# Optimization experiments

Measured on AMD Instinct MI355X. Metric: run time of the kernel, lower is better.

## Reference

```python
import jax, jax.numpy as jnp
import numpy as np
from jax import lax

HIDDEN = 256
CONV = 128
DIST = 11
GRID = DIST + 1            # 12
N_STAB = DIST * DIST - 1   # 120
N_LAYERS = 2
DILATIONS = tuple(min(2 ** i, DIST) for i in range(N_LAYERS))  # (1, 2)
EPS = 1e-5

# row-major placement of the first N_STAB grid cells (matches _build_grid_maps)
ROWS = jnp.arange(N_STAB) // GRID
COLS = jnp.arange(N_STAB) % GRID


def setup_inputs() -> dict:
    key = jax.random.key(0)
    ks = jax.random.split(key, 12)
    s_in = 1.0 / np.sqrt(HIDDEN)
    s_cv = 1.0 / np.sqrt(CONV * 9)
    s_out = 1.0 / np.sqrt(CONV)
    return {
        "x": jax.random.normal(ks[0], (4096, N_STAB, HIDDEN), jnp.float32),
        "W_in": jax.random.uniform(ks[1], (HIDDEN, CONV), jnp.float32, -s_in, s_in),
        "b_in": jax.random.uniform(ks[2], (CONV,), jnp.float32, -s_in, s_in),
        "conv_w": jax.random.uniform(ks[3], (N_LAYERS, CONV, CONV, 3, 3), jnp.float32, -s_cv, s_cv),
        "conv_b": jax.random.uniform(ks[4], (N_LAYERS, CONV), jnp.float32, -s_cv, s_cv),
        "bn_g": jnp.ones((N_LAYERS, CONV), jnp.float32),
        "bn_b": jnp.zeros((N_LAYERS, CONV), jnp.float32),
        "W_out": jax.random.uniform(ks[5], (CONV, HIDDEN), jnp.float32, -s_out, s_out),
        "b_out": jax.random.uniform(ks[6], (HIDDEN,), jnp.float32, -s_out, s_out),
        "ln_g": jnp.ones((HIDDEN,), jnp.float32),
        "ln_b": jnp.zeros((HIDDEN,), jnp.float32),
    }


def _dilated_conv(g, w, b, dil):
    # g: [B, C, G, G], w: [O, I, 3, 3]
    y = lax.conv_general_dilated(
        g, w, window_strides=(1, 1),
        padding=((dil, dil), (dil, dil)),
        rhs_dilation=(dil, dil),
        dimension_numbers=("NCHW", "OIHW", "NCHW"))
    return y + b[None, :, None, None]


def _batchnorm_train(y, gamma, beta):
    # training-mode BN: batch stats over (N, H, W), biased variance
    mean = jnp.mean(y, axis=(0, 2, 3), keepdims=True)
    var = jnp.mean(jnp.square(y - mean), axis=(0, 2, 3), keepdims=True)
    yhat = (y - mean) * lax.rsqrt(var + EPS)
    return yhat * gamma[None, :, None, None] + beta[None, :, None, None]


def reference(x, W_in, b_in, conv_w, conv_b, bn_g, bn_b, W_out, b_out, ln_g, ln_b):
    B = x.shape[0]
    # proj_in: [B, S, H] -> [B, S, C]
    h = jnp.einsum("bsh,hc->bsc", x, W_in) + b_in
    # scatter to grid: [B, C, G, G]
    grid = jnp.zeros((B, CONV, GRID, GRID), dtype=h.dtype)
    grid = grid.at[:, :, ROWS, COLS].set(jnp.transpose(h, (0, 2, 1)))
    for i, dil in enumerate(DILATIONS):
        y = _dilated_conv(grid, conv_w[i], conv_b[i], dil)
        grid = grid + jax.nn.relu(_batchnorm_train(y, bn_g[i], bn_b[i]))
    # gather back: [B, S, C]
    h = jnp.transpose(grid[:, :, ROWS, COLS], (0, 2, 1))
    # proj_out + residual + LayerNorm
    h = jnp.einsum("bsc,ch->bsh", h, W_out) + b_out
    z = x + h
    mu = jnp.mean(z, axis=-1, keepdims=True)
    var = jnp.mean(jnp.square(z - mu), axis=-1, keepdims=True)
    return (z - mu) * lax.rsqrt(var + EPS) * ln_g + ln_b
```

## Files before the change

### kernel.cpp

```cpp
#include <hip/hip_runtime.h>

typedef __attribute__((ext_vector_type(8))) unsigned short u16x8;
typedef __attribute__((ext_vector_type(8))) __bf16 bf16x8;
typedef __attribute__((ext_vector_type(4))) float f32x4;

#define DEVINL __device__ __forceinline__

DEVINL f32x4 MF(u16x8 a, u16x8 b, f32x4 c) {
  return __builtin_amdgcn_mfma_f32_16x16x32_bf16(
      __builtin_bit_cast(bf16x8, a), __builtin_bit_cast(bf16x8, b), c, 0, 0, 0);
}
DEVINL unsigned short f2b(float f) {
  return __builtin_bit_cast(unsigned short, (__bf16)f);
}
DEVINL float b2f(unsigned short h) {
  unsigned u = ((unsigned)h) << 16;
  return __builtin_bit_cast(float, u);
}

__global__ void k_prep(const float* __restrict__ W_in, const float* __restrict__ conv_w,
                       const float* __restrict__ W_out, unsigned short* __restrict__ Wt_in,
                       unsigned short* __restrict__ Wc, unsigned short* __restrict__ Wt_out) {
  int t = blockIdx.x * 256 + threadIdx.x;
  if (t < 128 * 256) { int c = t >> 8, h = t & 255; Wt_in[t] = f2b(W_in[h * 128 + c]); }
  if (t < 256 * 128) { int h = t >> 7, c = t & 127; Wt_out[t] = f2b(W_out[c * 256 + h]); }
  for (int i = t; i < 2 * 9 * 128 * 128; i += 65536) {
    int ii = i & 127, o = (i >> 7) & 127, rest = i >> 14;
    int kk = rest % 9, L = rest / 9;
    Wc[i] = f2b(conv_w[(size_t)((L * 128 + o) * 128 + ii) * 9 + kk]);
  }
}

DEVINL void conv_body(const char* GT, const unsigned short* __restrict__ WcL,
                      const float* __restrict__ convbL, int dil,
                      unsigned short* __restrict__ ybp, float* __restrict__ partials,
                      int b, int w, int hi, int lo) {
  const f32x4 Z = {0.f, 0.f, 0.f, 0.f};
  f32x4 acc[9][2];
#pragma unroll
  for (int mt = 0; mt < 9; ++mt) { acc[mt][0] = Z; acc[mt][1] = Z; }

  int pr[9], pc[9];
#pragma unroll
  for (int mt = 0; mt < 9; ++mt) {
    int p = mt * 16 + lo;
    pr[mt] = p / 12;
    pc[mt] = p - pr[mt] * 12;
  }

  for (int off = 0; off < 9; ++off) {
    const int dh = (off / 3 - 1) * dil, dw = (off % 3 - 1) * dil;
    int rb[9], sz[9];
#pragma unroll
    for (int mt = 0; mt < 9; ++mt) {
      int r2 = pr[mt] + dh, c2 = pc[mt] + dw;
      bool ok = ((unsigned)r2 < 12u) && ((unsigned)c2 < 12u);
      int ps = ok ? (r2 * 12 + c2) : 144;
      rb[mt] = ps * 256;
      sz[mt] = (ps & 7) << 4;
    }
    const unsigned short* Ao = WcL + off * (128 * 128);
#pragma unroll
    for (int ks = 0; ks < 4; ++ks) {
      const int kb = ks * 32 + hi * 8;
      u16x8 b0 = *(const u16x8*)(Ao + (w * 32 + lo) * 128 + kb);
      u16x8 b1 = *(const u16x8*)(Ao + (w * 32 + 16 + lo) * 128 + kb);
#pragma unroll
      for (int mt = 0; mt < 9; ++mt) {
        u16x8 a = *(const u16x8*)(GT + rb[mt] + ((kb * 2) ^ sz[mt]));
        acc[mt][0] = MF(a, b0, acc[mt][0]);
        acc[mt][1] = MF(a, b1, acc[mt][1]);
      }
    }
  }

  const float bias0 = convbL[w * 32 + lo], bias1 = convbL[w * 32 + 16 + lo];
  float s1a = 0.f, s2a = 0.f, s1b = 0.f, s2b = 0.f;
#pragma unroll
  for (int mt = 0; mt < 9; ++mt)
#pragma unroll
    for (int r = 0; r < 4; ++r) {
      const int p = mt * 16 + hi * 4 + r;
      float ya = acc[mt][0][r] + bias0;
      float yb = acc[mt][1][r] + bias1;
      s1a += ya; s2a += ya * ya; s1b += yb; s2b += yb * yb;
      ybp[p * 128 + w * 32 + lo]      = f2b(ya);
      ybp[p * 128 + w * 32 + 16 + lo] = f2b(yb);
    }
  s1a += __shfl_xor(s1a, 16); s1a += __shfl_xor(s1a, 32);
  s2a += __shfl_xor(s2a, 16); s2a += __shfl_xor(s2a, 32);
  s1b += __shfl_xor(s1b, 16); s1b += __shfl_xor(s1b, 32);
  s2b += __shfl_xor(s2b, 16); s2b += __shfl_xor(s2b, 32);
  if (hi == 0) {
    const int o0 = w * 32 + lo;
    partials[(size_t)o0 * 4096 + b]              = s1a;
    partials[(size_t)(128 + o0) * 4096 + b]      = s2a;
    partials[(size_t)(o0 + 16) * 4096 + b]       = s1b;
    partials[(size_t)(128 + o0 + 16) * 4096 + b] = s2b;
  }
}

__global__ __launch_bounds__(256) void k_in(
    const float* __restrict__ x, const unsigned short* __restrict__ Wt_in,
    const float* __restrict__ b_in, const unsigned short* __restrict__ Wc0,
    const float* __restrict__ convb0, unsigned short* __restrict__ gridb,
    unsigned short* __restrict__ ybuf, float* __restrict__ partials) {
  __shared__ unsigned short Gt[145 * 128];
  char* GT = (char*)Gt;
  const int b = blockIdx.x, t = threadIdx.x;
  const int l = t & 63, hi = l >> 4, lo = l & 15, w = t >> 6;
  const float* xb = x + (size_t)b * 120 * 256;

  const f32x4 Z = {0.f, 0.f, 0.f, 0.f};
  f32x4 acc[2][8];
#pragma unroll
  for (int mi = 0; mi < 2; ++mi)
#pragma unroll
    for (int cn = 0; cn < 8; ++cn) acc[mi][cn] = Z;

#pragma unroll
  for (int ks = 0; ks < 8; ++ks) {
    const int kb = ks * 32 + hi * 8;
    u16x8 af[2];
#pragma unroll
    for (int mi = 0; mi < 2; ++mi) {
      int s = w * 32 + mi * 16 + lo;
      s = s < 120 ? s : 119;
      const float* px = xb + s * 256 + kb;
      f32x4 v0 = *(const f32x4*)px;
      f32x4 v1 = *(const f32x4*)(px + 4);
      u16x8 a;
#pragma unroll
      for (int j = 0; j < 4; ++j) { a[j] = f2b(v0[j]); a[4 + j] = f2b(v1[j]); }
      af[mi] = a;
    }
#pragma unroll
    for (int cn = 0; cn < 8; ++cn) {
      u16x8 bf = *(const u16x8*)(Wt_in + (cn * 16 + lo) * 256 + kb);
      acc[0][cn] = MF(af[0], bf, acc[0][cn]);
      acc[1][cn] = MF(af[1], bf, acc[1][cn]);
    }
  }

  float binr[8];
#pragma unroll
  for (int cn = 0; cn < 8; ++cn) binr[cn] = b_in[cn * 16 + lo];

#pragma unroll
  for (int mi = 0; mi < 2; ++mi)
#pragma unroll
    for (int r = 0; r < 4; ++r) {
      const int s = w * 32 + mi * 16 + hi * 4 + r;
      if (s < 120) {
        const int sw = (s & 7) << 4;
#pragma unroll
        for (int cn = 0; cn < 8; ++cn) {
          const int cb = (cn * 16 + lo) * 2;
          *(unsigned short*)(GT + s * 256 + (cb ^ sw)) = f2b(acc[mi][cn][r] + binr[cn]);
        }
      }
    }
  {
    u16x8 zz = {0, 0, 0, 0, 0, 0, 0, 0};
    for (int idx = t; idx < 25 * 16; idx += 256) {
      int row = 120 + (idx >> 4), ch = (idx & 15) << 4;
      *(u16x8*)(GT + row * 256 + (ch ^ ((row & 7) << 4))) = zz;
    }
  }
  __syncthreads();

  unsigned short* gbp = gridb + (size_t)b * 144 * 128;
  for (int idx = t; idx < 144 * 16; idx += 256) {
    int row = idx >> 4, ch = (idx & 15) << 4;
    u16x8 v = *(const u16x8*)(GT + row * 256 + (ch ^ ((row & 7) << 4)));
    *(u16x8*)(gbp + row * 128 + ((idx & 15) << 3)) = v;
  }

  conv_body(GT, Wc0, convb0, 1, ybuf + (size_t)b * 144 * 128, partials, b, w, hi, lo);
}

__global__ __launch_bounds__(256) void k_conv2(
    unsigned short* __restrict__ gridb, unsigned short* __restrict__ ybuf,
    const float* __restrict__ statsP, const unsigned short* __restrict__ WcL,
    const float* __restrict__ convbL, float* __restrict__ partials) {
  __shared__ unsigned short Gt[145 * 128];
  char* GT = (char*)Gt;
  const int b = blockIdx.x, t = threadIdx.x;
  unsigned short* gbp = gridb + (size_t)b * 144 * 128;
  unsigned short* ybp = ybuf + (size_t)b * 144 * 128;
  const int c0 = (t & 15) * 8, prow = t >> 4;
  const f32x4 a0 = *(const f32x4*)(statsP + c0);
  const f32x4 a1 = *(const f32x4*)(statsP + c0 + 4);
  const f32x4 g0 = *(const f32x4*)(statsP + 128 + c0);
  const f32x4 g1 = *(const f32x4*)(statsP + 128 + c0 + 4);

#pragma unroll
  for (int it = 0; it < 9; ++it) {
    const int p = prow + 16 * it;
    u16x8 g = *(const u16x8*)(gbp + p * 128 + c0);
    u16x8 y = *(const u16x8*)(ybp + p * 128 + c0);
    u16x8 o;
#pragma unroll
    for (int j = 0; j < 4; ++j) {
      o[j]     = f2b(b2f(g[j])     + fmaxf(0.f, b2f(y[j])     * a0[j] + g0[j]));
      o[4 + j] = f2b(b2f(g[4 + j]) + fmaxf(0.f, b2f(y[4 + j]) * a1[j] + g1[j]));
    }
    *(u16x8*)(gbp + p * 128 + c0) = o;
    *(u16x8*)(GT + p * 256 + ((c0 * 2) ^ ((p & 7) << 4))) = o;
  }
  if (t < 16) {
    u16x8 zz = {0, 0, 0, 0, 0, 0, 0, 0};
    *(u16x8*)(GT + 144 * 256 + t * 16) = zz;
  }
  __syncthreads();

  conv_body(GT, WcL, convbL, 2, ybp, partials, b, t >> 6, (t & 63) >> 4, t & 15);
}

__global__ void k_stats(const float* __restrict__ partials, const float* __restrict__ bn_g,
                        const float* __restrict__ bn_b, float* __restrict__ statsL, float invN) {
  const int c = blockIdx.x, t = threadIdx.x;
  float s1 = 0.f, s2 = 0.f;
  const float* p1 = partials + (size_t)c * 4096;
  const float* p2 = partials + (size_t)(128 + c) * 4096;
  for (int j = t; j < 4096; j += 256) { s1 += p1[j]; s2 += p2[j]; }
#pragma unroll
  for (int m = 1; m < 64; m <<= 1) { s1 += __shfl_xor(s1, m); s2 += __shfl_xor(s2, m); }
  __shared__ float r1[4], r2[4];
  if ((t & 63) == 0) { r1[t >> 6] = s1; r2[t >> 6] = s2; }
  __syncthreads();
  if (t == 0) {
    float S1 = r1[0] + r1[1] + r1[2] + r1[3];
    float S2 = r2[0] + r2[1] + r2[2] + r2[3];
    float mean = S1 * invN;
    float var = fmaxf(S2 * invN - mean * mean, 0.f);
    float a = bn_g[c] * rsqrtf(var + 1e-5f);
    statsL[c] = a;
    statsL[128 + c] = bn_b[c] - mean * a;
  }
}

__global__ __launch_bounds__(512) void k_out(
    const unsigned short* __restrict__ gridb, const unsigned short* __restrict__ ybuf,
    const float* __restrict__ statsP, const unsigned short* __restrict__ Wt_out,
    const float* __restrict__ b_out, const float* __restrict__ x,
    const float* __restrict__ ln_g, const float* __restrict__ ln_b,
    float* __restrict__ out) {
  __shared__ unsigned short Gs[128 * 128];
  char* GT = (char*)Gs;
  const int b = blockIdx.x, t = threadIdx.x;
  const unsigned short* gbp = gridb + (size_t)b * 144 * 128;
  const unsigned short* ybp = ybuf + (size_t)b * 144 * 128;
  const int c0 = (t & 15) * 8, prow = t >> 4;
  const f32x4 a0 = *(const f32x4*)(statsP + c0);
  const f32x4 a1 = *(const f32x4*)(statsP + c0 + 4);
  const f32x4 g0 = *(const f32x4*)(statsP + 128 + c0);
  const f32x4 g1 = *(const f32x4*)(statsP + 128 + c0 + 4);

#pragma unroll
  for (int it = 0; it < 4; ++it) {
    const int p = prow + 32 * it;
    u16x8 o = {0, 0, 0, 0, 0, 0, 0, 0};
    if (p < 120) {
      u16x8 g = *(const u16x8*)(gbp + p * 128 + c0);
      u16x8 y = *(const u16x8*)(ybp + p * 128 + c0);
#pragma unroll
      for (int j = 0; j < 4; ++j) {
        o[j]     = f2b(b2f(g[j])     + fmaxf(0.f, b2f(y[j])     * a0[j] + g0[j]));
        o[4 + j] = f2b(b2f(g[4 + j]) + fmaxf(0.f, b2f(y[4 + j]) * a1[j] + g1[j]));
      }
    }
    *(u16x8*)(GT + p * 256 + ((c0 * 2) ^ ((p & 7) << 4))) = o;
  }
  __syncthreads();

  const int l = t & 63, hi = l >> 4, lo = l & 15, w = t >> 6;
  const f32x4 Z = {0.f, 0.f, 0.f, 0.f};
  f32x4 acc[16];
#pragma unroll
  for (int nt = 0; nt < 16; ++nt) acc[nt] = Z;

#pragma unroll
  for (int ks = 0; ks < 4; ++ks) {
    const int kb = ks * 32 + hi * 8;
    const int r0 = w * 16 + lo;
    u16x8 A0 = *(const u16x8*)(GT + r0 * 256 + ((kb * 2) ^ ((r0 & 7) << 4)));
#pragma unroll
    for (int q = 0; q < 4; ++q)
#pragma unroll
      for (int j = 0; j < 4; ++j) {
        const int R = q * 64 + lo * 4 + j;
        u16x8 bf = *(const u16x8*)(Wt_out + R * 128 + kb);
        acc[q * 4 + j] = MF(A0, bf, acc[q * 4 + j]);
      }
  }

  const float* xb = x + (size_t)b * 120 * 256;
  float* ob = out + (size_t)b * 120 * 256;
  f32x4 bo4[4];
#pragma unroll
  for (int q = 0; q < 4; ++q) bo4[q] = *(const f32x4*)(b_out + q * 64 + lo * 4);

#pragma unroll
  for (int r = 0; r < 4; ++r) {
    const int row = w * 16 + hi * 4 + r;
    if (row < 120) {
      float s1 = 0.f, s2 = 0.f;
#pragma unroll
      for (int q = 0; q < 4; ++q) {
        f32x4 xv = *(const f32x4*)(xb + row * 256 + q * 64 + lo * 4);
#pragma unroll
        for (int j = 0; j < 4; ++j) {
          float v = acc[q * 4 + j][r] + bo4[q][j] + xv[j];
          acc[q * 4 + j][r] = v;
          s1 += v; s2 += v * v;
        }
      }
#pragma unroll
      for (int m = 1; m < 16; m <<= 1) { s1 += __shfl_xor(s1, m); s2 += __shfl_xor(s2, m); }
      const float mu = s1 * (1.f / 256.f);
      const float var = fmaxf(s2 * (1.f / 256.f) - mu * mu, 0.f);
      const float rs = rsqrtf(var + 1e-5f);
#pragma unroll
      for (int q = 0; q < 4; ++q) {
        f32x4 lg = *(const f32x4*)(ln_g + q * 64 + lo * 4);
        f32x4 lb = *(const f32x4*)(ln_b + q * 64 + lo * 4);
        f32x4 o4;
#pragma unroll
        for (int j = 0; j < 4; ++j)
          o4[j] = (acc[q * 4 + j][r] - mu) * rs * lg[j] + lb[j];
        *(f32x4*)(ob + row * 256 + q * 64 + lo * 4) = o4;
      }
    }
  }
}

extern "C" void kernel_launch(void* const* d_in, const int* in_sizes, int n_in,
                              void* d_out, int out_size, void* d_ws, size_t ws_size,
                              hipStream_t stream) {
  (void)in_sizes; (void)n_in; (void)out_size; (void)ws_size;
  const float* x      = (const float*)d_in[0];
  const float* W_in   = (const float*)d_in[1];
  const float* b_in   = (const float*)d_in[2];
  const float* conv_w = (const float*)d_in[3];
  const float* conv_b = (const float*)d_in[4];
  const float* bn_g   = (const float*)d_in[5];
  const float* bn_b   = (const float*)d_in[6];
  const float* W_out  = (const float*)d_in[7];
  const float* b_out  = (const float*)d_in[8];
  const float* ln_g   = (const float*)d_in[9];
  const float* ln_b   = (const float*)d_in[10];

  char* ws = (char*)d_ws;
  size_t off = 0;
  auto alloc = [&](size_t bytes) { char* p = ws + off; off = (off + bytes + 255) & ~(size_t)255; return p; };
  unsigned short* Wt_in  = (unsigned short*)alloc(128 * 256 * 2);
  unsigned short* Wc     = (unsigned short*)alloc(2 * 9 * 128 * 128 * 2);
  unsigned short* Wt_out = (unsigned short*)alloc(256 * 128 * 2);
  float* stats           = (float*)alloc(2 * 256 * 4);
  float* partials        = (float*)alloc((size_t)256 * 4096 * 4);
  unsigned short* gridb  = (unsigned short*)alloc((size_t)4096 * 144 * 128 * 2);
  unsigned short* ybuf   = (unsigned short*)alloc((size_t)4096 * 144 * 128 * 2);

  const float invN = 1.f / (4096.f * 144.f);

  k_prep<<<256, 256, 0, stream>>>(W_in, conv_w, W_out, Wt_in, Wc, Wt_out);
  k_in<<<4096, 256, 0, stream>>>(x, Wt_in, b_in, Wc, conv_b, gridb, ybuf, partials);
  k_stats<<<128, 256, 0, stream>>>(partials, bn_g, bn_b, stats, invN);
  k_conv2<<<4096, 256, 0, stream>>>(gridb, ybuf, stats, Wc + 9 * 128 * 128, conv_b + 128, partials);
  k_stats<<<128, 256, 0, stream>>>(partials, bn_g + 128, bn_b + 128, stats + 256, invN);
  k_out<<<4096, 512, 0, stream>>>(gridb, ybuf, stats + 256, Wt_out, b_out, x, ln_g, ln_b, (float*)d_out);
}
```

Before: 1.139 ms.

## Split k_out into one-wave blocks per 16-row tile for finer scheduling

```diff
diff --git a/kernel.cpp b/kernel.cpp
--- a/kernel.cpp
+++ b/kernel.cpp
@@ -240,41 +240,54 @@
   }
 }
 
-__global__ __launch_bounds__(512) void k_out(
+__global__ __launch_bounds__(64, 4) void k_out(
     const unsigned short* __restrict__ gridb, const unsigned short* __restrict__ ybuf,
     const float* __restrict__ statsP, const unsigned short* __restrict__ Wt_out,
     const float* __restrict__ b_out, const float* __restrict__ x,
     const float* __restrict__ ln_g, const float* __restrict__ ln_b,
     float* __restrict__ out) {
-  __shared__ unsigned short Gs[128 * 128];
+  __shared__ unsigned short Gs[16 * 128];
   char* GT = (char*)Gs;
-  const int b = blockIdx.x, t = threadIdx.x;
+  const int bid = blockIdx.x;
+  const int b = bid >> 3, blk = bid & 7;
   const unsigned short* gbp = gridb + (size_t)b * 144 * 128;
   const unsigned short* ybp = ybuf + (size_t)b * 144 * 128;
-  const int c0 = (t & 15) * 8, prow = t >> 4;
-  const f32x4 a0 = *(const f32x4*)(statsP + c0);
-  const f32x4 a1 = *(const f32x4*)(statsP + c0 + 4);
-  const f32x4 g0 = *(const f32x4*)(statsP + 128 + c0);
-  const f32x4 g1 = *(const f32x4*)(statsP + 128 + c0 + 4);
-
-#pragma unroll
-  for (int it = 0; it < 4; ++it) {
-    const int p = prow + 32 * it;
-    u16x8 o = {0, 0, 0, 0, 0, 0, 0, 0};
+  const int t = threadIdx.x;
+
+  {
+    const int p_loc = t >> 2, c0 = (t & 3) * 32;
+    const int p = blk * 16 + p_loc;
+    const int sw = (p_loc & 7) << 4;
     if (p < 120) {
-      u16x8 g = *(const u16x8*)(gbp + p * 128 + c0);
-      u16x8 y = *(const u16x8*)(ybp + p * 128 + c0);
 #pragma unroll
       for (int j = 0; j < 4; ++j) {
-        o[j]     = f2b(b2f(g[j])     + fmaxf(0.f, b2f(y[j])     * a0[j] + g0[j]));
-        o[4 + j] = f2b(b2f(g[4 + j]) + fmaxf(0.f, b2f(y[4 + j]) * a1[j] + g1[j]));
-      }
-    }
-    *(u16x8*)(GT + p * 256 + ((c0 * 2) ^ ((p & 7) << 4))) = o;
+        const int c = c0 + j * 8;
+        u16x8 g = *(const u16x8*)(gbp + p * 128 + c);
+        u16x8 y = *(const u16x8*)(ybp + p * 128 + c);
+        const f32x4 a0 = *(const f32x4*)(statsP + c);
+        const f32x4 a1 = *(const f32x4*)(statsP + c + 4);
+        const f32x4 g0 = *(const f32x4*)(statsP + 128 + c);
+        const f32x4 g1 = *(const f32x4*)(statsP + 128 + c + 4);
+        u16x8 o;
+#pragma unroll
+        for (int k = 0; k < 4; ++k) {
+          o[k]     = f2b(b2f(g[k])     + fmaxf(0.f, b2f(y[k])     * a0[k] + g0[k]));
+          o[4 + k] = f2b(b2f(g[4 + k]) + fmaxf(0.f, b2f(y[4 + k]) * a1[k] + g1[k]));
+        }
+        *(u16x8*)(GT + p_loc * 256 + ((c * 2) ^ sw)) = o;
+      }
+    } else {
+      u16x8 zz = {0, 0, 0, 0, 0, 0, 0, 0};
+#pragma unroll
+      for (int j = 0; j < 4; ++j) {
+        const int c = c0 + j * 8;
+        *(u16x8*)(GT + p_loc * 256 + ((c * 2) ^ sw)) = zz;
+      }
+    }
   }
   __syncthreads();
 
-  const int l = t & 63, hi = l >> 4, lo = l & 15, w = t >> 6;
+  const int hi = t >> 4, lo = t & 15;
   const f32x4 Z = {0.f, 0.f, 0.f, 0.f};
   f32x4 acc[16];
 #pragma unroll
@@ -283,8 +296,7 @@
 #pragma unroll
   for (int ks = 0; ks < 4; ++ks) {
     const int kb = ks * 32 + hi * 8;
-    const int r0 = w * 16 + lo;
-    u16x8 A0 = *(const u16x8*)(GT + r0 * 256 + ((kb * 2) ^ ((r0 & 7) << 4)));
+    u16x8 A0 = *(const u16x8*)(GT + lo * 256 + ((kb * 2) ^ ((lo & 7) << 4)));
 #pragma unroll
     for (int q = 0; q < 4; ++q)
 #pragma unroll
@@ -303,7 +315,7 @@
 
 #pragma unroll
   for (int r = 0; r < 4; ++r) {
-    const int row = w * 16 + hi * 4 + r;
+    const int row = blk * 16 + hi * 4 + r;
     if (row < 120) {
       float s1 = 0.f, s2 = 0.f;
 #pragma unroll
@@ -369,5 +381,5 @@
   k_stats<<<128, 256, 0, stream>>>(partials, bn_g, bn_b, stats, invN);
   k_conv2<<<4096, 256, 0, stream>>>(gridb, ybuf, stats, Wc + 9 * 128 * 128, conv_b + 128, partials);
   k_stats<<<128, 256, 0, stream>>>(partials, bn_g + 128, bn_b + 128, stats + 256, invN);
-  k_out<<<4096, 512, 0, stream>>>(gridb, ybuf, stats + 256, Wt_out, b_out, x, ln_g, ln_b, (float*)d_out);
-}
+  k_out<<<4096 * 8, 64, 0, stream>>>(gridb, ybuf, stats + 256, Wt_out, b_out, x, ln_g, ln_b, (float*)d_out);
+}
```

Measured after the change: 1.136 ms. About the same (-0.3%).

## Recompute conv outputs in later kernels instead of storing intermediate buffers

Applied to the files above, without the earlier changes.

```diff
diff --git a/kernel.cpp b/kernel.cpp
--- a/kernel.cpp
+++ b/kernel.cpp
@@ -31,10 +31,10 @@
   }
 }
 
-DEVINL void conv_body(const char* GT, const unsigned short* __restrict__ WcL,
+template <int YMODE, bool PART>
+DEVINL void conv_body(const char* GT, char* YL, const unsigned short* __restrict__ WcL,
                       const float* __restrict__ convbL, int dil,
-                      unsigned short* __restrict__ ybp, float* __restrict__ partials,
-                      int b, int w, int hi, int lo) {
+                      float* __restrict__ partials, int b, int w, int hi, int lo) {
   const f32x4 Z = {0.f, 0.f, 0.f, 0.f};
   f32x4 acc[9][2];
 #pragma unroll
@@ -83,20 +83,61 @@
       const int p = mt * 16 + hi * 4 + r;
       float ya = acc[mt][0][r] + bias0;
       float yb = acc[mt][1][r] + bias1;
-      s1a += ya; s2a += ya * ya; s1b += yb; s2b += yb * yb;
-      ybp[p * 128 + w * 32 + lo]      = f2b(ya);
-      ybp[p * 128 + w * 32 + 16 + lo] = f2b(yb);
-    }
-  s1a += __shfl_xor(s1a, 16); s1a += __shfl_xor(s1a, 32);
-  s2a += __shfl_xor(s2a, 16); s2a += __shfl_xor(s2a, 32);
-  s1b += __shfl_xor(s1b, 16); s1b += __shfl_xor(s1b, 32);
-  s2b += __shfl_xor(s2b, 16); s2b += __shfl_xor(s2b, 32);
-  if (hi == 0) {
-    const int o0 = w * 32 + lo;
-    partials[(size_t)o0 * 4096 + b]              = s1a;
-    partials[(size_t)(128 + o0) * 4096 + b]      = s2a;
-    partials[(size_t)(o0 + 16) * 4096 + b]       = s1b;
-    partials[(size_t)(128 + o0 + 16) * 4096 + b] = s2b;
+      if (PART) { s1a += ya; s2a += ya * ya; s1b += yb; s2b += yb * yb; }
+      if (YMODE == 1) {
+        const int sw = (p & 7) << 4;
+        *(unsigned short*)(YL + p * 256 + ((((w * 32 + lo) * 2)) ^ sw))      = f2b(ya);
+        *(unsigned short*)(YL + p * 256 + ((((w * 32 + 16 + lo) * 2)) ^ sw)) = f2b(yb);
+      }
+    }
+  if (PART) {
+    s1a += __shfl_xor(s1a, 16); s1a += __shfl_xor(s1a, 32);
+    s2a += __shfl_xor(s2a, 16); s2a += __shfl_xor(s2a, 32);
+    s1b += __shfl_xor(s1b, 16); s1b += __shfl_xor(s1b, 32);
+    s2b += __shfl_xor(s2b, 16); s2b += __shfl_xor(s2b, 32);
+    if (hi == 0) {
+      const int o0 = w * 32 + lo;
+      partials[(size_t)o0 * 4096 + b]              = s1a;
+      partials[(size_t)(128 + o0) * 4096 + b]      = s2a;
+      partials[(size_t)(o0 + 16) * 4096 + b]       = s1b;
+      partials[(size_t)(128 + o0 + 16) * 4096 + b] = s2b;
+    }
+  }
+}
+
+DEVINL void stage_grid(const unsigned short* __restrict__ gbp, char* GT, int t) {
+  const int c0 = (t & 15) * 8, prow = t >> 4;
+#pragma unroll
+  for (int it = 0; it < 9; ++it) {
+    const int p = prow + 16 * it;
+    u16x8 g = *(const u16x8*)(gbp + p * 128 + c0);
+    *(u16x8*)(GT + p * 256 + ((c0 * 2) ^ ((p & 7) << 4))) = g;
+  }
+  if (t < 16) {
+    u16x8 zz = {0, 0, 0, 0, 0, 0, 0, 0};
+    *(u16x8*)(GT + 144 * 256 + t * 16) = zz;
+  }
+}
+
+DEVINL void bn_apply(char* GT, const char* YL, const float* __restrict__ statsP, int t) {
+  const int c0 = (t & 15) * 8, prow = t >> 4;
+  const f32x4 a0 = *(const f32x4*)(statsP + c0);
+  const f32x4 a1 = *(const f32x4*)(statsP + c0 + 4);
+  const f32x4 g0 = *(const f32x4*)(statsP + 128 + c0);
+  const f32x4 g1 = *(const f32x4*)(statsP + 128 + c0 + 4);
+#pragma unroll
+  for (int it = 0; it < 9; ++it) {
+    const int p = prow + 16 * it;
+    const int ad = p * 256 + ((c0 * 2) ^ ((p & 7) << 4));
+    u16x8 g = *(const u16x8*)(GT + ad);
+    u16x8 y = *(const u16x8*)(YL + ad);
+    u16x8 o;
+#pragma unroll
+    for (int j = 0; j < 4; ++j) {
+      o[j]     = f2b(b2f(g[j])     + fmaxf(0.f, b2f(y[j])     * a0[j] + g0[j]));
+      o[4 + j] = f2b(b2f(g[4 + j]) + fmaxf(0.f, b2f(y[4 + j]) * a1[j] + g1[j]));
+    }
+    *(u16x8*)(GT + ad) = o;
   }
 }
 
@@ -104,7 +145,7 @@
     const float* __restrict__ x, const unsigned short* __restrict__ Wt_in,
     const float* __restrict__ b_in, const unsigned short* __restrict__ Wc0,
     const float* __restrict__ convb0, unsigned short* __restrict__ gridb,
-    unsigned short* __restrict__ ybuf, float* __restrict__ partials) {
+    float* __restrict__ partials) {
   __shared__ unsigned short Gt[145 * 128];
   char* GT = (char*)Gt;
   const int b = blockIdx.x, t = threadIdx.x;
@@ -176,45 +217,28 @@
     *(u16x8*)(gbp + row * 128 + ((idx & 15) << 3)) = v;
   }
 
-  conv_body(GT, Wc0, convb0, 1, ybuf + (size_t)b * 144 * 128, partials, b, w, hi, lo);
-}
-
-__global__ __launch_bounds__(256) void k_conv2(
-    unsigned short* __restrict__ gridb, unsigned short* __restrict__ ybuf,
-    const float* __restrict__ statsP, const unsigned short* __restrict__ WcL,
-    const float* __restrict__ convbL, float* __restrict__ partials) {
+  conv_body<0, true>(GT, nullptr, Wc0, convb0, 1, partials, b, w, hi, lo);
+}
+
+__global__ __launch_bounds__(256) void k_mid(
+    const unsigned short* __restrict__ gridb, const float* __restrict__ stats1,
+    const unsigned short* __restrict__ Wc0, const float* __restrict__ convb0,
+    const unsigned short* __restrict__ Wc1, const float* __restrict__ convb1,
+    float* __restrict__ partials) {
   __shared__ unsigned short Gt[145 * 128];
+  __shared__ unsigned short Yl[144 * 128];
   char* GT = (char*)Gt;
+  char* YL = (char*)Yl;
   const int b = blockIdx.x, t = threadIdx.x;
-  unsigned short* gbp = gridb + (size_t)b * 144 * 128;
-  unsigned short* ybp = ybuf + (size_t)b * 144 * 128;
-  const int c0 = (t & 15) * 8, prow = t >> 4;
-  const f32x4 a0 = *(const f32x4*)(statsP + c0);
-  const f32x4 a1 = *(const f32x4*)(statsP + c0 + 4);
-  const f32x4 g0 = *(const f32x4*)(statsP + 128 + c0);
-  const f32x4 g1 = *(const f32x4*)(statsP + 128 + c0 + 4);
-
-#pragma unroll
-  for (int it = 0; it < 9; ++it) {
-    const int p = prow + 16 * it;
-    u16x8 g = *(const u16x8*)(gbp + p * 128 + c0);
-    u16x8 y = *(const u16x8*)(ybp + p * 128 + c0);
-    u16x8 o;
-#pragma unroll
-    for (int j = 0; j < 4; ++j) {
-      o[j]     = f2b(b2f(g[j])     + fmaxf(0.f, b2f(y[j])     * a0[j] + g0[j]));
-      o[4 + j] = f2b(b2f(g[4 + j]) + fmaxf(0.f, b2f(y[4 + j]) * a1[j] + g1[j]));
-    }
-    *(u16x8*)(gbp + p * 128 + c0) = o;
-    *(u16x8*)(GT + p * 256 + ((c0 * 2) ^ ((p & 7) << 4))) = o;
-  }
-  if (t < 16) {
-    u16x8 zz = {0, 0, 0, 0, 0, 0, 0, 0};
-    *(u16x8*)(GT + 144 * 256 + t * 16) = zz;
-  }
-  __syncthreads();
-
-  conv_body(GT, WcL, convbL, 2, ybp, partials, b, t >> 6, (t & 63) >> 4, t & 15);
+  const int l = t & 63, hi = l >> 4, lo = l & 15, w = t >> 6;
+
+  stage_grid(gridb + (size_t)b * 144 * 128, GT, t);
+  __syncthreads();
+  conv_body<1, false>(GT, YL, Wc0, convb0, 1, nullptr, b, w, hi, lo);
+  __syncthreads();
+  bn_apply(GT, YL, stats1, t);
+  __syncthreads();
+  conv_body<0, true>(GT, nullptr, Wc1, convb1, 2, partials, b, w, hi, lo);
 }
 
 __global__ void k_stats(const float* __restrict__ partials, const float* __restrict__ bn_g,
@@ -240,58 +264,53 @@
   }
 }
 
-__global__ __launch_bounds__(512) void k_out(
-    const unsigned short* __restrict__ gridb, const unsigned short* __restrict__ ybuf,
-    const float* __restrict__ statsP, const unsigned short* __restrict__ Wt_out,
-    const float* __restrict__ b_out, const float* __restrict__ x,
-    const float* __restrict__ ln_g, const float* __restrict__ ln_b,
-    float* __restrict__ out) {
-  __shared__ unsigned short Gs[128 * 128];
-  char* GT = (char*)Gs;
+__global__ __launch_bounds__(256) void k_out(
+    const unsigned short* __restrict__ gridb, const float* __restrict__ stats1,
+    const float* __restrict__ stats2,
+    const unsigned short* __restrict__ Wc0, const float* __restrict__ convb0,
+    const unsigned short* __restrict__ Wc1, const float* __restrict__ convb1,
+    const unsigned short* __restrict__ Wt_out, const float* __restrict__ b_out,
+    const float* __restrict__ x, const float* __restrict__ ln_g,
+    const float* __restrict__ ln_b, float* __restrict__ out) {
+  __shared__ unsigned short Gt[145 * 128];
+  __shared__ unsigned short Yl[144 * 128];
+  char* GT = (char*)Gt;
+  char* YL = (char*)Yl;
   const int b = blockIdx.x, t = threadIdx.x;
-  const unsigned short* gbp = gridb + (size_t)b * 144 * 128;
-  const unsigned short* ybp = ybuf + (size_t)b * 144 * 128;
-  const int c0 = (t & 15) * 8, prow = t >> 4;
-  const f32x4 a0 = *(const f32x4*)(statsP + c0);
-  const f32x4 a1 = *(const f32x4*)(statsP + c0 + 4);
-  const f32x4 g0 = *(const f32x4*)(statsP + 128 + c0);
-  const f32x4 g1 = *(const f32x4*)(statsP + 128 + c0 + 4);
-
-#pragma unroll
-  for (int it = 0; it < 4; ++it) {
-    const int p = prow + 32 * it;
-    u16x8 o = {0, 0, 0, 0, 0, 0, 0, 0};
-    if (p < 120) {
-      u16x8 g = *(const u16x8*)(gbp + p * 128 + c0);
-      u16x8 y = *(const u16x8*)(ybp + p * 128 + c0);
-#pragma unroll
-      for (int j = 0; j < 4; ++j) {
-        o[j]     = f2b(b2f(g[j])     + fmaxf(0.f, b2f(y[j])     * a0[j] + g0[j]));
-        o[4 + j] = f2b(b2f(g[4 + j]) + fmaxf(0.f, b2f(y[4 + j]) * a1[j] + g1[j]));
-      }
-    }
-    *(u16x8*)(GT + p * 256 + ((c0 * 2) ^ ((p & 7) << 4))) = o;
-  }
-  __syncthreads();
-
   const int l = t & 63, hi = l >> 4, lo = l & 15, w = t >> 6;
+
+  stage_grid(gridb + (size_t)b * 144 * 128, GT, t);
+  __syncthreads();
+  conv_body<1, false>(GT, YL, Wc0, convb0, 1, nullptr, b, w, hi, lo);
+  __syncthreads();
+  bn_apply(GT, YL, stats1, t);
+  __syncthreads();
+  conv_body<1, false>(GT, YL, Wc1, convb1, 2, nullptr, b, w, hi, lo);
+  __syncthreads();
+  bn_apply(GT, YL, stats2, t);
+  __syncthreads();
+
   const f32x4 Z = {0.f, 0.f, 0.f, 0.f};
-  f32x4 acc[16];
-#pragma unroll
-  for (int nt = 0; nt < 16; ++nt) acc[nt] = Z;
+  f32x4 acc[2][16];
+#pragma unroll
+  for (int mi = 0; mi < 2; ++mi)
+#pragma unroll
+    for (int nt = 0; nt < 16; ++nt) acc[mi][nt] = Z;
 
 #pragma unroll
   for (int ks = 0; ks < 4; ++ks) {
     const int kb = ks * 32 + hi * 8;
-    const int r0 = w * 16 + lo;
+    const int r0 = w * 32 + lo, r1 = r0 + 16;
     u16x8 A0 = *(const u16x8*)(GT + r0 * 256 + ((kb * 2) ^ ((r0 & 7) << 4)));
+    u16x8 A1 = *(const u16x8*)(GT + r1 * 256 + ((kb * 2) ^ ((r1 & 7) << 4)));
 #pragma unroll
     for (int q = 0; q < 4; ++q)
 #pragma unroll
       for (int j = 0; j < 4; ++j) {
         const int R = q * 64 + lo * 4 + j;
         u16x8 bf = *(const u16x8*)(Wt_out + R * 128 + kb);
-        acc[q * 4 + j] = MF(A0, bf, acc[q * 4 + j]);
+        acc[0][q * 4 + j] = MF(A0, bf, acc[0][q * 4 + j]);
+        acc[1][q * 4 + j] = MF(A1, bf, acc[1][q * 4 + j]);
       }
   }
 
@@ -302,37 +321,39 @@
   for (int q = 0; q < 4; ++q) bo4[q] = *(const f32x4*)(b_out + q * 64 + lo * 4);
 
 #pragma unroll
-  for (int r = 0; r < 4; ++r) {
-    const int row = w * 16 + hi * 4 + r;
-    if (row < 120) {
-      float s1 = 0.f, s2 = 0.f;
-#pragma unroll
-      for (int q = 0; q < 4; ++q) {
-        f32x4 xv = *(const f32x4*)(xb + row * 256 + q * 64 + lo * 4);
-#pragma unroll
-        for (int j = 0; j < 4; ++j) {
-          float v = acc[q * 4 + j][r] + bo4[q][j] + xv[j];
-          acc[q * 4 + j][r] = v;
-          s1 += v; s2 += v * v;
+  for (int mi = 0; mi < 2; ++mi)
+#pragma unroll
+    for (int r = 0; r < 4; ++r) {
+      const int row = w * 32 + mi * 16 + hi * 4 + r;
+      if (row < 120) {
+        float s1 = 0.f, s2 = 0.f;
+#pragma unroll
+        for (int q = 0; q < 4; ++q) {
+          f32x4 xv = *(const f32x4*)(xb + row * 256 + q * 64 + lo * 4);
+#pragma unroll
+          for (int j = 0; j < 4; ++j) {
+            float v = acc[mi][q * 4 + j][r] + bo4[q][j] + xv[j];
+            acc[mi][q * 4 + j][r] = v;
+            s1 += v; s2 += v * v;
+          }
         }
-      }
-#pragma unroll
-      for (int m = 1; m < 16; m <<= 1) { s1 += __shfl_xor(s1, m); s2 += __shfl_xor(s2, m); }
-      const float mu = s1 * (1.f / 256.f);
-      const float var = fmaxf(s2 * (1.f / 256.f) - mu * mu, 0.f);
-      const float rs = rsqrtf(var + 1e-5f);
-#pragma unroll
-      for (int q = 0; q < 4; ++q) {
-        f32x4 lg = *(const f32x4*)(ln_g + q * 64 + lo * 4);
-        f32x4 lb = *(const f32x4*)(ln_b + q * 64 + lo * 4);
-        f32x4 o4;
-#pragma unroll
-        for (int j = 0; j < 4; ++j)
-          o4[j] = (acc[q * 4 + j][r] - mu) * rs * lg[j] + lb[j];
-        *(f32x4*)(ob + row * 256 + q * 64 + lo * 4) = o4;
-      }
-    }
-  }
+#pragma unroll
+        for (int m = 1; m < 16; m <<= 1) { s1 += __shfl_xor(s1, m); s2 += __shfl_xor(s2, m); }
+        const float mu = s1 * (1.f / 256.f);
+        const float var = fmaxf(s2 * (1.f / 256.f) - mu * mu, 0.f);
+        const float rs = rsqrtf(var + 1e-5f);
+#pragma unroll
+        for (int q = 0; q < 4; ++q) {
+          f32x4 lg = *(const f32x4*)(ln_g + q * 64 + lo * 4);
+          f32x4 lb = *(const f32x4*)(ln_b + q * 64 + lo * 4);
+          f32x4 o4;
+#pragma unroll
+          for (int j = 0; j < 4; ++j)
+            o4[j] = (acc[mi][q * 4 + j][r] - mu) * rs * lg[j] + lb[j];
+          *(f32x4*)(ob + row * 256 + q * 64 + lo * 4) = o4;
+        }
+      }
+    }
 }
 
 extern "C" void kernel_launch(void* const* d_in, const int* in_sizes, int n_in,
@@ -360,14 +381,15 @@
   float* stats           = (float*)alloc(2 * 256 * 4);
   float* partials        = (float*)alloc((size_t)256 * 4096 * 4);
   unsigned short* gridb  = (unsigned short*)alloc((size_t)4096 * 144 * 128 * 2);
-  unsigned short* ybuf   = (unsigned short*)alloc((size_t)4096 * 144 * 128 * 2);
 
   const float invN = 1.f / (4096.f * 144.f);
+  const unsigned short* Wc1 = Wc + 9 * 128 * 128;
 
   k_prep<<<256, 256, 0, stream>>>(W_in, conv_w, W_out, Wt_in, Wc, Wt_out);
-  k_in<<<4096, 256, 0, stream>>>(x, Wt_in, b_in, Wc, conv_b, gridb, ybuf, partials);
+  k_in<<<4096, 256, 0, stream>>>(x, Wt_in, b_in, Wc, conv_b, gridb, partials);
   k_stats<<<128, 256, 0, stream>>>(partials, bn_g, bn_b, stats, invN);
-  k_conv2<<<4096, 256, 0, stream>>>(gridb, ybuf, stats, Wc + 9 * 128 * 128, conv_b + 128, partials);
+  k_mid<<<4096, 256, 0, stream>>>(gridb, stats, Wc, conv_b, Wc1, conv_b + 128, partials);
   k_stats<<<128, 256, 0, stream>>>(partials, bn_g + 128, bn_b + 128, stats + 256, invN);
-  k_out<<<4096, 512, 0, stream>>>(gridb, ybuf, stats + 256, Wt_out, b_out, x, ln_g, ln_b, (float*)d_out);
-}
+  k_out<<<4096, 256, 0, stream>>>(gridb, stats, stats + 256, Wc, conv_b, Wc1, conv_b + 128,
+                                  Wt_out, b_out, x, ln_g, ln_b, (float*)d_out);
+}
```

After: 1.742 ms. 52.9% more time.
